# Optimization experiments

Hardware: AMD Instinct MI355X
Metric: run time of the kernel (lower is better)

## Reference

```python
import math
import jax, jax.numpy as jnp
import numpy as np

B, N, M = 8, 1024, 32
D = 128      # node_dim
E = 32       # edge_dim
DD = 32      # dist_dim
MSG = 128    # message_dim
P = 128      # proj_dim
THETA = 10000.0


def _linear(x, w, b):
    return x @ w + b


def _sinusoidal(t, dim, theta=THETA):
    half = dim // 2
    freqs = jnp.exp(jnp.arange(half, dtype=t.dtype) * (-math.log(theta) / (half - 1)))
    ang = t[..., None] * freqs  # (..., half)
    return jnp.concatenate([jnp.sin(ang), jnp.cos(ang)], axis=-1)


def setup_inputs() -> dict:
    key = jax.random.key(0)
    ks = jax.random.split(key, 20)
    pair_in = 2 * D + E + DD  # NUM_ATOMS == 1

    def w(k, shape):
        fan_in = shape[0]
        return jax.random.uniform(k, shape, jnp.float32, -1, 1) / np.sqrt(fan_in)

    return {
        "embeddings": jax.random.normal(ks[0], (B, N, D), jnp.float32),
        "coords": jax.random.normal(ks[1], (B, N, 3), jnp.float32),
        "padding_mask": jnp.ones((B, N), jnp.float32),
        "edges": jax.random.normal(ks[2], (B, N, M, E), jnp.float32),
        "we_w1": w(ks[3], (pair_in, MSG)), "we_b1": jnp.zeros((MSG,), jnp.float32),
        "we_w2": w(ks[4], (MSG, MSG)),    "we_b2": jnp.zeros((MSG,), jnp.float32),
        "wx_w1": w(ks[5], (MSG, P)),      "wx_b1": jnp.zeros((P,), jnp.float32),
        "wx_w2": w(ks[6], (P, 1)),        "wx_b2": jnp.zeros((1,), jnp.float32),
        "wh_w1": w(ks[7], (D + MSG, P)),  "wh_b1": jnp.zeros((P,), jnp.float32),
        "wh_w2": w(ks[8], (P, D)),        "wh_b2": jnp.zeros((D,), jnp.float32),
        "neighbor_ids": jax.random.randint(ks[9], (B, N, M), 0, N),
    }


def _gather(x, idx):
    # x: (B, N, d), idx: (B, N, M) -> (B, N, M, d). Direct gather,
    # mathematically identical to the one-hot einsum in the original.
    Bx, Nx, d = x.shape
    flat = jnp.take_along_axis(x, idx.reshape(Bx, -1, 1), axis=1)
    return flat.reshape(Bx, Nx, idx.shape[-1], d)


def reference(embeddings, coords, padding_mask, edges,
              we_w1, we_b1, we_w2, we_b2,
              wx_w1, wx_b1, wx_w2, wx_b2,
              wh_w1, wh_b1, wh_w2, wh_b2,
              neighbor_ids):
    feats2 = _gather(embeddings, neighbor_ids)          # (B,N,M,D)
    n_coords = _gather(coords, neighbor_ids)            # (B,N,M,3)
    rel_coors = coords[:, :, None, :] - n_coords        # (B,N,M,3)
    rel_dist = jnp.linalg.norm(rel_coors, axis=-1)      # (B,N,M)
    dists = _sinusoidal(rel_dist, DD)                   # (B,N,M,DD)

    feats1 = jnp.broadcast_to(embeddings[:, :, None, :], feats2.shape)
    feats_pair = jnp.concatenate([feats1, feats2, dists, edges], axis=-1)

    h = jax.nn.relu(_linear(feats_pair, we_w1, we_b1))
    m_ij = _linear(h, we_w2, we_b2)                     # (B,N,M,MSG)

    # coordinate update (unit vectors are detached in the original)
    unit = jax.lax.stop_gradient(
        jnp.nan_to_num(rel_coors / rel_dist[..., None]))
    px = _linear(jax.nn.relu(_linear(m_ij, wx_w1, wx_b1)), wx_w2, wx_b2)
    coords_out = coords + (unit * px).sum(axis=2) / M

    # feature update
    m_masked = m_ij * padding_mask[:, :, None, None]
    m_i = m_masked.sum(axis=2) / M                      # (B,N,MSG)
    hh = jnp.concatenate([embeddings, m_i], axis=-1)
    ph = _linear(jax.nn.relu(_linear(hh, wh_w1, wh_b1)), wh_w2, wh_b2)
    embeddings_out = embeddings + ph

    return embeddings_out, coords_out
```

## Files before the change

kernel.cpp:

```cpp
#include <hip/hip_runtime.h>
#include <hip/hip_bf16.h>

typedef __hip_bfloat16 bf16;
typedef short short8 __attribute__((ext_vector_type(8)));
typedef float f32x4 __attribute__((ext_vector_type(4)));
typedef int   int4v __attribute__((ext_vector_type(4)));

#define NB 8
#define NN 1024
#define NM 32
#define ND 128
#define NE 32
#define NODES (NB*NN)
#define NPB 4
#define NR  (NPB*NM)

#define OFF_W1AT   0
#define OFF_W1BT   32768
#define OFF_W1CDT  65536
#define OFF_W2T    81920
#define OFF_WX1T   114688
#define OFF_WH1AT  147456
#define OFF_WH1BT  180224
#define OFF_WH2T   212992
#define OFF_W2XT   245760
#define OFF_W2HT   278528
#define OFF_B2X    311296
#define OFF_B2H    311808
#define OFF_Y1     312320
#define OFF_Y2     (OFF_Y1 + 2097152)
#define NEED_FAST  ((size_t)OFF_Y2 + 2097152)

__device__ __forceinline__ float toF(bf16 x){ return __bfloat162float(x); }
__device__ __forceinline__ bf16  toB(float x){ return __float2bfloat16(x); }
__device__ __forceinline__ float rawF(short s){
  bf16 b; __builtin_memcpy(&b, &s, 2); return __bfloat162float(b);
}

__device__ __forceinline__ void bar_lds(){
  asm volatile("s_waitcnt lgkmcnt(0)" ::: "memory");
  __builtin_amdgcn_s_barrier();
}

__device__ __forceinline__ short8 pin8(short8 w){
  union { short8 s; int4v i; } u; u.s = w;
  asm volatile("" : "+v"(u.i));
  return u.s;
}

__device__ __forceinline__ void cp16f(bf16* d, const float* s){
  #pragma unroll
  for (int q = 0; q < 4; ++q){
    float4 a = ((const float4*)s)[q];
    d[q*4+0]=toB(a.x); d[q*4+1]=toB(a.y); d[q*4+2]=toB(a.z); d[q*4+3]=toB(a.w);
  }
}
__device__ __forceinline__ void cp8f(bf16* d, const float* s){
  #pragma unroll
  for (int q = 0; q < 2; ++q){
    float4 a = ((const float4*)s)[q];
    d[q*4+0]=toB(a.x); d[q*4+1]=toB(a.y); d[q*4+2]=toB(a.z); d[q*4+3]=toB(a.w);
  }
}
__device__ __forceinline__ void cp4f(bf16* d, const float* s){
  float4 a = *(const float4*)s;
  d[0]=toB(a.x); d[1]=toB(a.y); d[2]=toB(a.z); d[3]=toB(a.w);
}

#define MFMA(a,b,c) __builtin_amdgcn_mfma_f32_16x16x32_bf16((a),(b),(c),0,0,0)

__global__ __launch_bounds__(256) void k_trc(const float* __restrict__ w1,
    const float* __restrict__ w2, const float* __restrict__ wx1,
    const float* __restrict__ wh1, const float* __restrict__ wh2,
    const float* __restrict__ b2, const float* __restrict__ bx1,
    char* __restrict__ ws){
  const int blk = blockIdx.x;
  const int tid = threadIdx.x;
  if (blk < 480){
    int i = blk*256 + tid;
    const float* src; int koff, KT, dst, e;
    if      (i <  16384){ src=w1;  koff=0;   KT=128; dst=OFF_W1AT;  e=i; }
    else if (i <  32768){ src=w1;  koff=128; KT=128; dst=OFF_W1BT;  e=i-16384; }
    else if (i <  40960){ src=w1;  koff=256; KT=64;  dst=OFF_W1CDT; e=i-32768; }
    else if (i <  57344){ src=w2;  koff=0;   KT=128; dst=OFF_W2T;   e=i-40960; }
    else if (i <  73728){ src=wx1; koff=0;   KT=128; dst=OFF_WX1T;  e=i-57344; }
    else if (i <  90112){ src=wh1; koff=0;   KT=128; dst=OFF_WH1AT; e=i-73728; }
    else if (i < 106496){ src=wh1; koff=128; KT=128; dst=OFF_WH1BT; e=i-90112; }
    else               { src=wh2; koff=0;   KT=128; dst=OFF_WH2T;  e=i-106496; }
    int c = e / KT, k = e - c*KT;
    ((bf16*)(ws+dst))[e] = toB(src[(size_t)(koff+k)*128 + c]);
    return;
  }
  if (blk == 512){
    const int k = tid;
    if (k < 128){
      float bx = 0.f, bh = 0.f;
      for (int q = 0; q < 128; ++q){
        const float b2q = b2[q];
        bx += b2q * wx1[q*128 + k];
        bh += b2q * wh1[(size_t)(128+q)*128 + k];
      }
      ((float*)(ws+OFF_B2X))[k] = bx + bx1[k];
      ((float*)(ws+OFF_B2H))[k] = bh;
    }
    return;
  }
  const int bid2 = blk - 480;
  const int part = bid2 >> 4;
  const int sub2 = bid2 & 15;
  const int r0   = (sub2 >> 1) * 16;
  const int ch   = sub2 & 1;
  const float* A = part ? (wh1 + 128*128) : wx1;
  bf16* OUT = (bf16*)(ws + (part ? OFF_W2HT : OFF_W2XT));
  const int lane = tid & 63, wv = tid >> 6, lr = lane & 15, lk = lane >> 4;
  const int kcol = ch*64 + wv*16 + lr;
  f32x4 acc = {};
  #pragma unroll
  for (int kc = 0; kc < 4; ++kc){
    const int q0 = kc*32 + lk*8;
    short8 a, b;
    #pragma unroll
    for (int i = 0; i < 8; ++i){
      bf16 ta = toB(A[(size_t)(q0+i)*128 + r0 + lr]);
      bf16 tb = toB(w2[(size_t)kcol*128 + q0 + i]);
      short sa, sb; __builtin_memcpy(&sa,&ta,2); __builtin_memcpy(&sb,&tb,2);
      a[i] = sa; b[i] = sb;
    }
    acc = MFMA(a, b, acc);
  }
  #pragma unroll
  for (int r = 0; r < 4; ++r)
    OUT[(size_t)(r0 + lk*4 + r)*128 + kcol] = toB(acc[r]);
}

__global__ __launch_bounds__(256) void k_prep(const float* __restrict__ emb,
    const float* __restrict__ eb1, char* __restrict__ ws){
  __shared__ __align__(16) bf16 sE[32][136];
  const int tid = threadIdx.x, g0 = blockIdx.x*32;
  { const int row = tid >> 3, sub = tid & 7;
    cp16f(&sE[row][sub*16], emb + (size_t)(g0+row)*ND + sub*16); }
  bar_lds();
  const int lane = tid & 63, wv = tid >> 6, lr = lane & 15, lk = lane >> 4;
  const int c0 = wv*16 + lr, c1 = (wv+4)*16 + lr;
  const short* wt[2] = {(const short*)(ws+OFF_W1AT), (const short*)(ws+OFF_W1BT)};
  bf16* yo[2] = {(bf16*)(ws+OFF_Y1), (bf16*)(ws+OFF_Y2)};
  #pragma unroll
  for (int t = 0; t < 2; ++t){
    f32x4 acc[2][2] = {};
    #pragma unroll
    for (int kc = 0; kc < 4; ++kc){
      const int k0 = kc*32 + lk*8;
      short8 a0 = *(const short8*)&sE[lr][k0];
      short8 a1 = *(const short8*)&sE[16+lr][k0];
      short8 w0 = *(const short8*)&wt[t][c0*128 + k0];
      short8 w1v= *(const short8*)&wt[t][c1*128 + k0];
      acc[0][0]=MFMA(a0,w0,acc[0][0]);  acc[1][0]=MFMA(a1,w0,acc[1][0]);
      acc[0][1]=MFMA(a0,w1v,acc[0][1]); acc[1][1]=MFMA(a1,w1v,acc[1][1]);
    }
    const float b0 = (t==0) ? eb1[c0] : 0.f;
    const float b1 = (t==0) ? eb1[c1] : 0.f;
    #pragma unroll
    for (int rt = 0; rt < 2; ++rt)
      #pragma unroll
      for (int r = 0; r < 4; ++r){
        const int orow = rt*16 + lk*4 + r;
        const size_t g = (size_t)(g0 + orow)*ND;
        yo[t][g + c0] = toB(acc[rt][0][r] + b0);
        yo[t][g + c1] = toB(acc[rt][1][r] + b1);
      }
  }
}

__global__ __launch_bounds__(512) void k_edges_fast(
    const float* __restrict__ coords, const float* __restrict__ mask,
    const float* __restrict__ edges,  const float* __restrict__ xw2,
    const float* __restrict__ xb2,    const int* __restrict__ nids,
    const char* __restrict__ ws,      float* __restrict__ out)
{
  const short* w1cdT = (const short*)(ws+OFF_W1CDT);
  const short* w2xT  = (const short*)(ws+OFF_W2XT);
  const bf16*  Y1    = (const bf16*)(ws+OFF_Y1);
  const bf16*  Y2    = (const bf16*)(ws+OFF_Y2);
  const float* B2X   = (const float*)(ws+OFF_B2X);

  __shared__ __align__(16) char regA[NR*136*2];
  __shared__ __align__(16) bf16 sH[NR][136];
  __shared__ float sUnit[NR][3];
  __shared__ float sPx[NR];
  bf16 (*sDE)[72]  = (bf16(*)[72])regA;
  bf16 (*sX)[136]  = (bf16(*)[136])regA;

  const int bid = blockIdx.x;
  const int nbk = ((bid & 7) << 8) + (bid >> 3);
  const int g0  = nbk * NPB;
  const int bi  = g0 >> 10;
  const int tid = threadIdx.x;
  const int lane = tid & 63, wv = tid >> 6;
  const int lr = lane & 15, lk = lane >> 4;
  const int c0 = wv*16 + lr;

  short8 rw1[2], rwx[4];
  #pragma unroll
  for (int kc = 0; kc < 2; ++kc)
    rw1[kc] = pin8(*(const short8*)&w1cdT[c0*64 + kc*32 + lk*8]);
  #pragma unroll
  for (int kc = 0; kc < 4; ++kc)
    rwx[kc] = pin8(*(const short8*)&w2xT[c0*128 + kc*32 + lk*8]);
  const float bxc  = B2X[c0];
  const float wxc  = xw2[c0];
  const float bx2v = xb2[0];
  float mv[NPB];
  #pragma unroll
  for (int n = 0; n < NPB; ++n) mv[n] = mask[g0+n];

  {
    const int row = tid >> 2, sub = tid & 3;
    const int node = row >> 5;
    const int j = nids[(size_t)(g0+node)*NM + (row & 31)];
    const float* cs = coords + (size_t)(g0+node)*3;
    const float* cj = coords + ((size_t)bi*NN + j)*3;
    const float rx = cs[0]-cj[0], ry = cs[1]-cj[1], rz = cs[2]-cj[2];
    const float d2 = rx*rx + ry*ry + rz*rz;
    const float dist = sqrtf(d2);
    if (sub == 0){
      const float inv = (d2 > 0.f) ? 1.f/dist : 0.f;
      sUnit[row][0]=rx*inv; sUnit[row][1]=ry*inv; sUnit[row][2]=rz*inv;
    }
    cp8f(&sDE[row][32 + sub*8],
         edges + ((size_t)(g0+node)*NM + (row&31))*NE + sub*8);
    #pragma unroll
    for (int q = 0; q < 8; ++q){
      const int dd = sub*8 + q, h = dd & 15;
      const float ang = dist * __expf(-0.6140226909f * (float)h);
      sDE[row][dd] = toB((dd < 16) ? __sinf(ang) : __cosf(ang));
    }
    const bf16* y1p = Y1 + (size_t)(g0+node)*ND + sub*32;
    const bf16* y2p = Y2 + ((size_t)bi*NN + j)*ND + sub*32;
    #pragma unroll
    for (int h8 = 0; h8 < 4; ++h8){
      short8 a = *(const short8*)(y1p + h8*8);
      short8 b = *(const short8*)(y2p + h8*8);
      short8 o;
      #pragma unroll
      for (int q = 0; q < 8; ++q){
        bf16 rsum = toB(rawF(a[q]) + rawF(b[q]));
        short sr; __builtin_memcpy(&sr,&rsum,2);
        o[q] = sr;
      }
      *(short8*)&sH[row][sub*32 + h8*8] = o;
    }
  }
  bar_lds();

  {
    float hsum[NPB] = {};
    #pragma unroll
    for (int t = 0; t < 8; ++t){
      f32x4 acc = {};
      #pragma unroll
      for (int kc = 0; kc < 2; ++kc){
        short8 a = *(const short8*)&sDE[t*16 + lr][kc*32 + lk*8];
        acc = MFMA(a, rw1[kc], acc);
      }
      #pragma unroll
      for (int r = 0; r < 4; ++r){
        const int orow = t*16 + lk*4 + r;
        const float hv = fmaxf(toF(sH[orow][c0]) + acc[r], 0.f);
        sH[orow][c0] = toB(hv);
        hsum[t>>1] += hv;
      }
    }
    #pragma unroll
    for (int n = 0; n < NPB; ++n){
      hsum[n] += __shfl_xor(hsum[n], 16);
      hsum[n] += __shfl_xor(hsum[n], 32);
    }
    if (lk == 0){
      #pragma unroll
      for (int n = 0; n < NPB; ++n)
        out[(size_t)(g0+n)*ND + c0] = hsum[n] * mv[n] * (1.f/32.f);
    }
  }
  bar_lds();

  {
    #pragma unroll
    for (int t = 0; t < 8; ++t){
      f32x4 acc = {};
      #pragma unroll
      for (int kc = 0; kc < 4; ++kc){
        short8 a = *(const short8*)&sH[t*16 + lr][kc*32 + lk*8];
        acc = MFMA(a, rwx[kc], acc);
      }
      #pragma unroll
      for (int r = 0; r < 4; ++r){
        const int orow = t*16 + lk*4 + r;
        sX[orow][c0] = toB(fmaxf(acc[r] + bxc, 0.f) * wxc);
      }
    }
  }
  bar_lds();

  {
    const int row = tid >> 2, sub = tid & 3;
    float p = 0.f;
    #pragma unroll
    for (int c8 = 0; c8 < 4; ++c8){
      short8 x = *(const short8*)&sX[row][sub*32 + c8*8];
      #pragma unroll
      for (int q = 0; q < 8; ++q) p += rawF(x[q]);
    }
    p += __shfl_xor(p, 1); p += __shfl_xor(p, 2);
    if (sub == 0) sPx[row] = p + bx2v;
  }
  bar_lds();

  if (tid < NR){
    const float px = sPx[tid];
    float v0 = sUnit[tid][0]*px, v1 = sUnit[tid][1]*px, v2 = sUnit[tid][2]*px;
    #pragma unroll
    for (int m = 1; m < 32; m <<= 1){
      v0 += __shfl_xor(v0, m);
      v1 += __shfl_xor(v1, m);
      v2 += __shfl_xor(v2, m);
    }
    const int node = tid >> 5, d = tid & 31;
    if (d < 3){
      const float s = (d==0) ? v0 : (d==1 ? v1 : v2);
      out[(size_t)NODES*ND + (size_t)(g0+node)*3 + d] =
          coords[(size_t)(g0+node)*3 + d] + s*(1.f/32.f);
    }
  }
}

__global__ __launch_bounds__(256) void k_edges_compact(
    const float* __restrict__ emb,   const float* __restrict__ coords,
    const float* __restrict__ mask,  const float* __restrict__ edges,
    const float* __restrict__ eb1,   const float* __restrict__ eb2,
    const float* __restrict__ xb1,   const float* __restrict__ xw2,
    const float* __restrict__ xb2,   const int* __restrict__ nids,
    const char* __restrict__ ws,     float* __restrict__ out)
{
  const short* w1aT  = (const short*)(ws+OFF_W1AT);
  const short* w1bT  = (const short*)(ws+OFF_W1BT);
  const short* w1cdT = (const short*)(ws+OFF_W1CDT);
  const short* w2T   = (const short*)(ws+OFF_W2T);
  const short* wx1T  = (const short*)(ws+OFF_WX1T);

  __shared__ __align__(16) bf16 sA[32][336];
  __shared__ __align__(16) bf16 sH[32][136];
  __shared__ __align__(16) bf16 sM[32][136];
  __shared__ float sUnit[32][3];
  __shared__ float sPx[32];
  __shared__ int   sIds[32];
  __shared__ float sSelfC[3];

  const int tid = threadIdx.x;
  const int nb  = blockIdx.x;
  const int bi  = nb >> 10;

  if (tid < 32) sIds[tid] = nids[nb*NM + tid];
  if (tid < 3)  sSelfC[tid] = coords[(size_t)nb*3 + tid];
  __syncthreads();

  {
    const int row = tid >> 3, sub = tid & 7;
    const int j = sIds[row];
    cp16f(&sA[row][sub*16],       emb + (size_t)nb*ND + sub*16);
    cp16f(&sA[row][128 + sub*16], emb + ((size_t)bi*NN + j)*ND + sub*16);
    cp4f (&sA[row][288 + sub*4],  edges + ((size_t)nb*NM + row)*NE + sub*4);
    float jx = coords[((size_t)bi*NN + j)*3 + 0];
    float jy = coords[((size_t)bi*NN + j)*3 + 1];
    float jz = coords[((size_t)bi*NN + j)*3 + 2];
    float rx = sSelfC[0]-jx, ry = sSelfC[1]-jy, rz = sSelfC[2]-jz;
    float d2 = rx*rx + ry*ry + rz*rz;
    float dist = sqrtf(d2);
    if (sub == 0){
      float inv = (d2 > 0.f) ? 1.f/dist : 0.f;
      sUnit[row][0]=rx*inv; sUnit[row][1]=ry*inv; sUnit[row][2]=rz*inv;
    }
    #pragma unroll
    for (int q = 0; q < 4; ++q){
      const int dd = sub*4 + q, h = dd & 15;
      float ang = dist * __expf(-0.6140226909f * (float)h);
      sA[row][256+dd] = toB((dd < 16) ? __sinf(ang) : __cosf(ang));
    }
  }
  __syncthreads();

  const int lane = tid & 63, wv = tid >> 6, lr = lane & 15, lk = lane >> 4;
  const int c0 = wv*16 + lr, c1 = (wv+4)*16 + lr;

  {
    f32x4 acc[2][2] = {};
    #pragma unroll
    for (int kc = 0; kc < 10; ++kc){
      const int k0 = kc*32 + lk*8;
      const short* wp; int kk, KT;
      if (kc < 4){ wp = w1aT; kk = k0; KT = 128; }
      else if (kc < 8){ wp = w1bT; kk = k0-128; KT = 128; }
      else { wp = w1cdT; kk = k0-256; KT = 64; }
      short8 a0 = *(const short8*)&sA[lr][k0];
      short8 a1 = *(const short8*)&sA[16+lr][k0];
      short8 w0 = *(const short8*)&wp[c0*KT + kk];
      short8 w1v= *(const short8*)&wp[c1*KT + kk];
      acc[0][0]=MFMA(a0,w0,acc[0][0]);  acc[1][0]=MFMA(a1,w0,acc[1][0]);
      acc[0][1]=MFMA(a0,w1v,acc[0][1]); acc[1][1]=MFMA(a1,w1v,acc[1][1]);
    }
    const float b0 = eb1[c0], b1 = eb1[c1];
    #pragma unroll
    for (int rt = 0; rt < 2; ++rt)
      #pragma unroll
      for (int r = 0; r < 4; ++r){
        const int orow = rt*16 + lk*4 + r;
        sH[orow][c0] = toB(fmaxf(acc[rt][0][r]+b0, 0.f));
        sH[orow][c1] = toB(fmaxf(acc[rt][1][r]+b1, 0.f));
      }
  }
  __syncthreads();

  {
    f32x4 acc[2][2] = {};
    #pragma unroll
    for (int kc = 0; kc < 4; ++kc){
      const int k0 = kc*32 + lk*8;
      short8 a0 = *(const short8*)&sH[lr][k0];
      short8 a1 = *(const short8*)&sH[16+lr][k0];
      short8 w0 = *(const short8*)&w2T[c0*128 + k0];
      short8 w1v= *(const short8*)&w2T[c1*128 + k0];
      acc[0][0]=MFMA(a0,w0,acc[0][0]);  acc[1][0]=MFMA(a1,w0,acc[1][0]);
      acc[0][1]=MFMA(a0,w1v,acc[0][1]); acc[1][1]=MFMA(a1,w1v,acc[1][1]);
    }
    const float b0 = eb2[c0], b1 = eb2[c1];
    #pragma unroll
    for (int rt = 0; rt < 2; ++rt)
      #pragma unroll
      for (int r = 0; r < 4; ++r){
        const int orow = rt*16 + lk*4 + r;
        sM[orow][c0] = toB(acc[rt][0][r] + b0);
        sM[orow][c1] = toB(acc[rt][1][r] + b1);
      }
  }
  __syncthreads();

  {
    f32x4 acc[2][2] = {};
    #pragma unroll
    for (int kc = 0; kc < 4; ++kc){
      const int k0 = kc*32 + lk*8;
      short8 a0 = *(const short8*)&sM[lr][k0];
      short8 a1 = *(const short8*)&sM[16+lr][k0];
      short8 w0 = *(const short8*)&wx1T[c0*128 + k0];
      short8 w1v= *(const short8*)&wx1T[c1*128 + k0];
      acc[0][0]=MFMA(a0,w0,acc[0][0]);  acc[1][0]=MFMA(a1,w0,acc[1][0]);
      acc[0][1]=MFMA(a0,w1v,acc[0][1]); acc[1][1]=MFMA(a1,w1v,acc[1][1]);
    }
    const float b0 = xb1[c0], b1 = xb1[c1];
    #pragma unroll
    for (int rt = 0; rt < 2; ++rt)
      #pragma unroll
      for (int r = 0; r < 4; ++r){
        const int orow = rt*16 + lk*4 + r;
        sH[orow][c0] = toB(fmaxf(acc[rt][0][r]+b0, 0.f));
        sH[orow][c1] = toB(fmaxf(acc[rt][1][r]+b1, 0.f));
      }
  }
  __syncthreads();

  {
    const int row = tid >> 3, sub = tid & 7;
    float p = 0.f;
    #pragma unroll
    for (int q = 0; q < 16; ++q){
      const int c = sub*16 + q;
      p += toF(sH[row][c]) * xw2[c];
    }
    p += __shfl_down(p,4,8); p += __shfl_down(p,2,8); p += __shfl_down(p,1,8);
    if (sub == 0) sPx[row] = p + xb2[0];
  }
  if (tid < 128){
    float s = 0.f;
    #pragma unroll
    for (int m = 0; m < 32; ++m) s += toF(sM[m][tid]);
    out[(size_t)nb*ND + tid] = s * mask[nb] * (1.f/32.f);
  }
  __syncthreads();
  if (tid < 3){
    float s = 0.f;
    #pragma unroll
    for (int m = 0; m < 32; ++m) s += sUnit[m][tid]*sPx[m];
    out[(size_t)NODES*ND + (size_t)nb*3 + tid] = sSelfC[tid] + s*(1.f/32.f);
  }
}

template<int HB>
__global__ __launch_bounds__(256) void k_node(
    const float* __restrict__ emb, const float* __restrict__ mask,
    const float* __restrict__ hb1, const float* __restrict__ hb2,
    const char* __restrict__ ws, float* __restrict__ out)
{
  const short* whaT = (const short*)(ws+OFF_WH1AT);
  const short* whbT = (const short*)(ws + (HB ? OFF_W2HT : OFF_WH1BT));
  const short* wh2T = (const short*)(ws+OFF_WH2T);
  const float* b2h  = (const float*)(ws+OFF_B2H);
  __shared__ __align__(16) bf16 sE[32][136];
  __shared__ __align__(16) bf16 sM[32][136];
  __shared__ __align__(16) bf16 sH[32][136];
  __shared__ float sMask[32];
  const int tid = threadIdx.x, g0 = blockIdx.x*32;
  const int lane = tid & 63, wv = tid >> 6, lr = lane & 15, lk = lane >> 4;
  const int c0 = wv*16 + lr, c1 = (wv+4)*16 + lr;

  short8 rwa[2][4], rwb[2][4], rw2[2][4];
  #pragma unroll
  for (int kc = 0; kc < 4; ++kc){
    rwa[0][kc] = *(const short8*)&whaT[c0*128 + kc*32 + lk*8];
    rwa[1][kc] = *(const short8*)&whaT[c1*128 + kc*32 + lk*8];
    rwb[0][kc] = *(const short8*)&whbT[c0*128 + kc*32 + lk*8];
    rwb[1][kc] = *(const short8*)&whbT[c1*128 + kc*32 + lk*8];
    rw2[0][kc] = *(const short8*)&wh2T[c0*128 + kc*32 + lk*8];
    rw2[1][kc] = *(const short8*)&wh2T[c1*128 + kc*32 + lk*8];
  }
  const float b1c0 = hb1[c0], b1c1 = hb1[c1];
  const float b2c0 = hb2[c0], b2c1 = hb2[c1];
  const float bhc0 = HB ? b2h[c0] : 0.f;
  const float bhc1 = HB ? b2h[c1] : 0.f;

  { const int row = tid >> 3, sub = tid & 7;
    cp16f(&sE[row][sub*16], emb + (size_t)(g0+row)*ND + sub*16);
    cp16f(&sM[row][sub*16], out + (size_t)(g0+row)*ND + sub*16); }
  if (tid < 32) sMask[tid] = mask[g0 + tid];
  bar_lds();
  {
    f32x4 acc[2][2] = {};
    #pragma unroll
    for (int kc = 0; kc < 4; ++kc){
      const int k0 = kc*32 + lk*8;
      short8 a0 = *(const short8*)&sE[lr][k0];
      short8 a1 = *(const short8*)&sE[16+lr][k0];
      acc[0][0]=MFMA(a0,rwa[0][kc],acc[0][0]); acc[1][0]=MFMA(a1,rwa[0][kc],acc[1][0]);
      acc[0][1]=MFMA(a0,rwa[1][kc],acc[0][1]); acc[1][1]=MFMA(a1,rwa[1][kc],acc[1][1]);
    }
    #pragma unroll
    for (int kc = 0; kc < 4; ++kc){
      const int k0 = kc*32 + lk*8;
      short8 a0 = *(const short8*)&sM[lr][k0];
      short8 a1 = *(const short8*)&sM[16+lr][k0];
      acc[0][0]=MFMA(a0,rwb[0][kc],acc[0][0]); acc[1][0]=MFMA(a1,rwb[0][kc],acc[1][0]);
      acc[0][1]=MFMA(a0,rwb[1][kc],acc[0][1]); acc[1][1]=MFMA(a1,rwb[1][kc],acc[1][1]);
    }
    #pragma unroll
    for (int rt = 0; rt < 2; ++rt)
      #pragma unroll
      for (int r = 0; r < 4; ++r){
        const int orow = rt*16 + lk*4 + r;
        const float mk = HB ? sMask[orow] : 0.f;
        sH[orow][c0] = toB(fmaxf(acc[rt][0][r] + b1c0 + mk*bhc0, 0.f));
        sH[orow][c1] = toB(fmaxf(acc[rt][1][r] + b1c1 + mk*bhc1, 0.f));
      }
  }
  bar_lds();
  {
    f32x4 acc[2][2] = {};
    #pragma unroll
    for (int kc = 0; kc < 4; ++kc){
      const int k0 = kc*32 + lk*8;
      short8 a0 = *(const short8*)&sH[lr][k0];
      short8 a1 = *(const short8*)&sH[16+lr][k0];
      acc[0][0]=MFMA(a0,rw2[0][kc],acc[0][0]); acc[1][0]=MFMA(a1,rw2[0][kc],acc[1][0]);
      acc[0][1]=MFMA(a0,rw2[1][kc],acc[0][1]); acc[1][1]=MFMA(a1,rw2[1][kc],acc[1][1]);
    }
    #pragma unroll
    for (int rt = 0; rt < 2; ++rt)
      #pragma unroll
      for (int r = 0; r < 4; ++r){
        const int orow = rt*16 + lk*4 + r;
        const size_t g = (size_t)(g0 + orow)*ND;
        out[g + c0] = acc[rt][0][r] + b2c0 + emb[g + c0];
        out[g + c1] = acc[rt][1][r] + b2c1 + emb[g + c1];
      }
  }
}

extern "C" void kernel_launch(void* const* d_in, const int* in_sizes, int n_in,
                              void* d_out, int out_size, void* d_ws, size_t ws_size,
                              hipStream_t stream) {
  const float* emb    = (const float*)d_in[0];
  const float* coords = (const float*)d_in[1];
  const float* mask   = (const float*)d_in[2];
  const float* edges  = (const float*)d_in[3];
  const float* we_w1  = (const float*)d_in[4];
  const float* we_b1  = (const float*)d_in[5];
  const float* we_w2  = (const float*)d_in[6];
  const float* we_b2  = (const float*)d_in[7];
  const float* wx_w1  = (const float*)d_in[8];
  const float* wx_b1  = (const float*)d_in[9];
  const float* wx_w2  = (const float*)d_in[10];
  const float* wx_b2  = (const float*)d_in[11];
  const float* wh_w1  = (const float*)d_in[12];
  const float* wh_b1  = (const float*)d_in[13];
  const float* wh_w2  = (const float*)d_in[14];
  const float* wh_b2  = (const float*)d_in[15];
  const int*   nids   = (const int*)d_in[16];
  float* out = (float*)d_out;
  char* ws = (char*)d_ws;
  const bool fast = (ws_size >= NEED_FAST);

  k_trc<<<(fast ? 513 : 480),256,0,stream>>>(we_w1, we_w2, wx_w1, wh_w1,
      wh_w2, we_b2, wx_b1, ws);

  if (fast){
    k_prep<<<NODES/32,256,0,stream>>>(emb, we_b1, ws);
    k_edges_fast<<<NODES/NPB,512,0,stream>>>(coords, mask, edges,
        wx_w2, wx_b2, nids, ws, out);
    k_node<1><<<NODES/32,256,0,stream>>>(emb, mask, wh_b1, wh_b2, ws, out);
  } else {
    k_edges_compact<<<NODES,256,0,stream>>>(emb, coords, mask, edges,
        we_b1, we_b2, wx_b1, wx_w2, wx_b2, nids, ws, out);
    k_node<0><<<NODES/32,256,0,stream>>>(emb, mask, wh_b1, wh_b2, ws, out);
  }
}
```

Before: 62.04 us.

## Fuse node-update MLP into edge kernel epilogue, dropping k_node launch

Moves the per-node feature-update MLP (wh_w1/wh_w2) into the tail of k_edges_fast. The per-node message sum now stays in shared memory as bf16 instead of being written to global and re-read by a separate kernel, which also removes one launch. The cost is that each block handles only 4 nodes padded to a 16-row MFMA tile, so it reloads the node-MLP weights from global per block with mostly wasted rows. The fused kernel also needs extra LDS and an extra barrier, and the intermediate m_i is now rounded to bf16.

```diff
diff --git a/kernel.cpp b/kernel.cpp
--- a/kernel.cpp
+++ b/kernel.cpp
@@ -172,23 +172,29 @@
 }
 
 __global__ __launch_bounds__(512) void k_edges_fast(
-    const float* __restrict__ coords, const float* __restrict__ mask,
-    const float* __restrict__ edges,  const float* __restrict__ xw2,
-    const float* __restrict__ xb2,    const int* __restrict__ nids,
-    const char* __restrict__ ws,      float* __restrict__ out)
+    const float* __restrict__ emb,    const float* __restrict__ coords,
+    const float* __restrict__ mask,   const float* __restrict__ edges,
+    const float* __restrict__ xw2,    const float* __restrict__ xb2,
+    const float* __restrict__ hb1,    const float* __restrict__ hb2,
+    const int* __restrict__ nids,     const char* __restrict__ ws,
+    float* __restrict__ out)
 {
   const short* w1cdT = (const short*)(ws+OFF_W1CDT);
   const short* w2xT  = (const short*)(ws+OFF_W2XT);
   const bf16*  Y1    = (const bf16*)(ws+OFF_Y1);
   const bf16*  Y2    = (const bf16*)(ws+OFF_Y2);
   const float* B2X   = (const float*)(ws+OFF_B2X);
+  const float* B2H   = (const float*)(ws+OFF_B2H);
 
   __shared__ __align__(16) char regA[NR*136*2];
   __shared__ __align__(16) bf16 sH[NR][136];
+  __shared__ __align__(16) bf16 sE[16][136];
+  __shared__ __align__(16) bf16 sHb[16][136];
   __shared__ float sUnit[NR][3];
   __shared__ float sPx[NR];
   bf16 (*sDE)[72]  = (bf16(*)[72])regA;
   bf16 (*sX)[136]  = (bf16(*)[136])regA;
+  bf16 (*sP)[136]  = (bf16(*)[136])regA;
 
   const int bid = blockIdx.x;
   const int nbk = ((bid & 7) << 8) + (bid >> 3);
@@ -249,6 +255,7 @@
       }
       *(short8*)&sH[row][sub*32 + h8*8] = o;
     }
+    sE[tid >> 7][tid & 127] = toB(emb[(size_t)(g0 + (tid >> 7))*ND + (tid & 127)]);
   }
   bar_lds();
 
@@ -278,7 +285,7 @@
     if (lk == 0){
       #pragma unroll
       for (int n = 0; n < NPB; ++n)
-        out[(size_t)(g0+n)*ND + c0] = hsum[n] * mv[n] * (1.f/32.f);
+        sHb[n][c0] = toB(hsum[n] * mv[n] * (1.f/32.f));
     }
   }
   bar_lds();
@@ -329,6 +336,52 @@
       const float s = (d==0) ? v0 : (d==1 ? v1 : v2);
       out[(size_t)NODES*ND + (size_t)(g0+node)*3 + d] =
           coords[(size_t)(g0+node)*3 + d] + s*(1.f/32.f);
+    }
+  }
+  {
+    const short* whaT = (const short*)(ws+OFF_WH1AT);
+    const short* w2hT = (const short*)(ws+OFF_W2HT);
+    f32x4 acc = {};
+    #pragma unroll
+    for (int kc = 0; kc < 4; ++kc){
+      const int k0 = kc*32 + lk*8;
+      short8 a = *(const short8*)&sE[lr][k0];
+      short8 w = *(const short8*)&whaT[c0*128 + k0];
+      acc = MFMA(a, w, acc);
+    }
+    #pragma unroll
+    for (int kc = 0; kc < 4; ++kc){
+      const int k0 = kc*32 + lk*8;
+      short8 a = *(const short8*)&sHb[lr][k0];
+      short8 w = *(const short8*)&w2hT[c0*128 + k0];
+      acc = MFMA(a, w, acc);
+    }
+    if (lk == 0){
+      const float b1c = hb1[c0], bhc = B2H[c0];
+      #pragma unroll
+      for (int r = 0; r < 4; ++r)
+        sP[r][c0] = toB(fmaxf(acc[r] + b1c + mv[r]*bhc, 0.f));
+    }
+  }
+  bar_lds();
+
+  {
+    const short* wh2T = (const short*)(ws+OFF_WH2T);
+    f32x4 acc = {};
+    #pragma unroll
+    for (int kc = 0; kc < 4; ++kc){
+      const int k0 = kc*32 + lk*8;
+      short8 a = *(const short8*)&sP[lr][k0];
+      short8 w = *(const short8*)&wh2T[c0*128 + k0];
+      acc = MFMA(a, w, acc);
+    }
+    if (lk == 0){
+      const float b2c = hb2[c0];
+      #pragma unroll
+      for (int r = 0; r < 4; ++r){
+        const size_t g = (size_t)(g0 + r)*ND;
+        out[g + c0] = acc[r] + b2c + emb[g + c0];
+      }
     }
   }
 }
@@ -493,20 +546,17 @@
   }
 }
 
-template<int HB>
 __global__ __launch_bounds__(256) void k_node(
     const float* __restrict__ emb, const float* __restrict__ mask,
     const float* __restrict__ hb1, const float* __restrict__ hb2,
     const char* __restrict__ ws, float* __restrict__ out)
 {
   const short* whaT = (const short*)(ws+OFF_WH1AT);
-  const short* whbT = (const short*)(ws + (HB ? OFF_W2HT : OFF_WH1BT));
+  const short* whbT = (const short*)(ws+OFF_WH1BT);
   const short* wh2T = (const short*)(ws+OFF_WH2T);
-  const float* b2h  = (const float*)(ws+OFF_B2H);
   __shared__ __align__(16) bf16 sE[32][136];
   __shared__ __align__(16) bf16 sM[32][136];
   __shared__ __align__(16) bf16 sH[32][136];
-  __shared__ float sMask[32];
   const int tid = threadIdx.x, g0 = blockIdx.x*32;
   const int lane = tid & 63, wv = tid >> 6, lr = lane & 15, lk = lane >> 4;
   const int c0 = wv*16 + lr, c1 = (wv+4)*16 + lr;
@@ -523,13 +573,10 @@
   }
   const float b1c0 = hb1[c0], b1c1 = hb1[c1];
   const float b2c0 = hb2[c0], b2c1 = hb2[c1];
-  const float bhc0 = HB ? b2h[c0] : 0.f;
-  const float bhc1 = HB ? b2h[c1] : 0.f;
 
   { const int row = tid >> 3, sub = tid & 7;
     cp16f(&sE[row][sub*16], emb + (size_t)(g0+row)*ND + sub*16);
     cp16f(&sM[row][sub*16], out + (size_t)(g0+row)*ND + sub*16); }
-  if (tid < 32) sMask[tid] = mask[g0 + tid];
   bar_lds();
   {
     f32x4 acc[2][2] = {};
@@ -554,9 +601,8 @@
       #pragma unroll
       for (int r = 0; r < 4; ++r){
         const int orow = rt*16 + lk*4 + r;
-        const float mk = HB ? sMask[orow] : 0.f;
-        sH[orow][c0] = toB(fmaxf(acc[rt][0][r] + b1c0 + mk*bhc0, 0.f));
-        sH[orow][c1] = toB(fmaxf(acc[rt][1][r] + b1c1 + mk*bhc1, 0.f));
+        sH[orow][c0] = toB(fmaxf(acc[rt][0][r] + b1c0, 0.f));
+        sH[orow][c1] = toB(fmaxf(acc[rt][1][r] + b1c1, 0.f));
       }
   }
   bar_lds();
@@ -611,12 +657,11 @@
 
   if (fast){
     k_prep<<<NODES/32,256,0,stream>>>(emb, we_b1, ws);
-    k_edges_fast<<<NODES/NPB,512,0,stream>>>(coords, mask, edges,
-        wx_w2, wx_b2, nids, ws, out);
-    k_node<1><<<NODES/32,256,0,stream>>>(emb, mask, wh_b1, wh_b2, ws, out);
+    k_edges_fast<<<NODES/NPB,512,0,stream>>>(emb, coords, mask, edges,
+        wx_w2, wx_b2, wh_b1, wh_b2, nids, ws, out);
   } else {
     k_edges_compact<<<NODES,256,0,stream>>>(emb, coords, mask, edges,
         we_b1, we_b2, wx_b1, wx_w2, wx_b2, nids, ws, out);
-    k_node<0><<<NODES/32,256,0,stream>>>(emb, mask, wh_b1, wh_b2, ws, out);
-  }
-}
+    k_node<<<NODES/32,256,0,stream>>>(emb, mask, wh_b1, wh_b2, ws, out);
+  }
+}
```

Measured after the change: 76.09 us. 1.23x slower.
